# Kernel optimization log

Hardware: AMD Instinct MI355X
Metric: run time of the kernel (lower is better)

Reference implementation:

```python
import jax, jax.numpy as jnp
import numpy as np

B, D, TC, TE, TGT = 8, 256, 2048, 2048, 256
SCALE = 16.0  # sqrt(256.0) hardcoded in the original module


def setup_inputs() -> dict:
    key = jax.random.key(0)
    k1, k2, k3 = jax.random.split(key, 3)
    content_emb = jax.random.normal(k1, (B, D, TC), dtype=jnp.float32)
    emotion_emb = jax.random.normal(k2, (B, D, TE), dtype=jnp.float32)
    # Conv1d(embed_dim*2 -> target_embed, kernel=3): weight [out, in, k]
    fan_in = 2 * D * 3
    conv_w = jax.random.normal(k3, (TGT, 2 * D, 3), dtype=jnp.float32) / np.sqrt(fan_in)
    conv_b = jnp.zeros((TGT,), dtype=jnp.float32)
    return {"content_emb": content_emb, "emotion_emb": emotion_emb,
            "conv_w": conv_w, "conv_b": conv_b}


def reference(content_emb, emotion_emb, conv_w, conv_b):
    # (B, D, T) -> (B, T, D)
    c = jnp.transpose(content_emb, (0, 2, 1))   # [B, Tc, D]
    e = jnp.transpose(emotion_emb, (0, 2, 1))   # [B, Te, D]
    sim = jnp.einsum('btd,bsd->bts', c, e)      # [B, Tc, Te]
    attn = jax.nn.softmax(sim / SCALE, axis=-1)
    weighted_emo = jnp.einsum('bts,bsd->btd', attn, e)  # [B, Tc, D]
    x = jnp.concatenate([c, weighted_emo], axis=-1)     # [B, Tc, 2D]
    x = jnp.transpose(x, (0, 2, 1))                     # [B, 2D, Tc]
    out = jax.lax.conv_general_dilated(
        x, conv_w, window_strides=(1,), padding=[(1, 1)],
        dimension_numbers=('NCH', 'OIH', 'NCH'))
    return out + conv_b[None, :, None]
```

## Files before the change

### kernel.cpp

```cpp
#include <hip/hip_runtime.h>

typedef __bf16 bf16x8 __attribute__((ext_vector_type(8)));
typedef __bf16 bf16x4 __attribute__((ext_vector_type(4)));
typedef float  f32x4  __attribute__((ext_vector_type(4)));

#define MFMA(a, b, c) __builtin_amdgcn_mfma_f32_16x16x32_bf16((a), (b), (c), 0, 0, 0)
#define DRAIN_VMCNT() __builtin_amdgcn_s_waitcnt(0x0F70)

constexpr int Bc  = 8;
constexpr int D   = 256;
constexpr int TC  = 2048;
constexpr int TE  = 2048;
constexpr int TGT = 256;
constexpr int XR  = 256;
constexpr int NBT = Bc * TC;

#define EXP_C 0.09016844005556021f

__device__ __forceinline__ void gl_lds16(const __bf16* g, __bf16* l) {
  __builtin_amdgcn_global_load_lds(
      (const __attribute__((address_space(1))) void*)g,
      (__attribute__((address_space(3))) void*)l, 16, 0, 0);
}

__global__ void k_prep_all(const float* __restrict__ content,
                           const float* __restrict__ emotion,
                           __bf16* __restrict__ xcat,
                           __bf16* __restrict__ e_t, __bf16* __restrict__ e_ds,
                           const float* __restrict__ w, __bf16* __restrict__ Wk) {
  __shared__ __bf16 tile[64][68];
  const int tid = threadIdx.x;

  if (blockIdx.x == TC / 64) {
    const int base = (blockIdx.y * Bc + blockIdx.z) * 2048;
#pragma unroll
    for (int j = 0; j < 8; ++j) {
      const int idx = base + j * 256 + tid;
      const int o = idx >> 9, i = idx & 511;
#pragma unroll
      for (int k = 0; k < 3; ++k)
        Wk[k * (TGT * 512) + idx] = (__bf16)w[(size_t)o * 1536 + i * 3 + k];
    }
    return;
  }

  const bool isC = blockIdx.y < 4;
  const int b  = blockIdx.z;
  const int t0 = blockIdx.x * 64;
  const int d0 = (blockIdx.y & 3) * 64;
  const int c4 = (tid & 15) * 4;
  const int r0 = tid >> 4;
  const float* sp = (isC ? content : emotion) + ((size_t)b * D + d0) * 2048 + t0;
  __bf16* dsp = e_ds + ((size_t)b * D + d0) * TE + t0;
#pragma unroll
  for (int i = 0; i < 4; ++i) {
    const int r = r0 + 16 * i;
    const float4 v = *(const float4*)(sp + (size_t)r * 2048 + c4);
    bf16x4 pv;
    pv[0] = (__bf16)v.x; pv[1] = (__bf16)v.y; pv[2] = (__bf16)v.z; pv[3] = (__bf16)v.w;
    *(bf16x4*)&tile[r][c4] = pv;
    if (!isC) *(bf16x4*)(dsp + (size_t)r * TE + c4) = pv;
  }
  __syncthreads();
  __bf16* dp = (isC ? xcat + ((size_t)b * TC + t0) * XR
                    : e_t + ((size_t)b * TE + t0) * D) + d0;
#pragma unroll
  for (int i = 0; i < 2; ++i) {
    const int idx = tid + 256 * i;
    const int r   = idx >> 3;
    const int c8  = (idx & 7) * 8;
    bf16x8 v;
#pragma unroll
    for (int j = 0; j < 8; ++j) v[j] = tile[c8 + j][r];
    *(bf16x8*)(dp + (size_t)r * 256 + c8) = v;
  }
}

__global__ __launch_bounds__(256, 2) void k_attn(const __bf16* __restrict__ xcat,
                                                 const __bf16* __restrict__ e_t,
                                                 const __bf16* __restrict__ e_ds,
                                                 __bf16* __restrict__ Op,
                                                 float* __restrict__ Lp) {
  __shared__ __align__(16) __bf16 sEt[2][8192];
  __shared__ __align__(16) __bf16 sEs[2][8192];
  __shared__ __align__(16) __bf16 sP[4][2][640];

  const int tid  = threadIdx.x;
  const int lane = tid & 63;
  const int w    = tid >> 6;
  const int q    = lane >> 4;
  const int tl   = lane & 15;
  const int b    = blockIdx.y;
  const int z    = blockIdx.z;
  const int tbase = blockIdx.x * 128 + w * 32;

  const __bf16* etb = e_t  + (size_t)b * TE * D;
  const __bf16* esb = e_ds + (size_t)b * D * TE;

  bf16x8 cB[2][8];
#pragma unroll
  for (int tt = 0; tt < 2; ++tt) {
    const __bf16* crow = xcat + ((size_t)(b * TC) + tbase + tt * 16 + tl) * XR + q * 8;
#pragma unroll
    for (int ks = 0; ks < 8; ++ks) cB[tt][ks] = *(const bf16x8*)(crow + ks * 32);
  }

  unsigned offEt[4], offEs[4];
#pragma unroll
  for (int c = 0; c < 4; ++c) {
    const int id = (w * 4 + c) * 64 + lane;
    const int ss = id >> 5, cs = id & 31;
    offEt[c] = ss * D + (cs ^ (ss & 7)) * 8;
    const int dd = id >> 2, ps = id & 3;
    offEs[c] = dd * TE + (ps ^ ((dd >> 2) & 3)) * 8;
  }

  f32x4 accO[2][16];
#pragma unroll
  for (int tt = 0; tt < 2; ++tt)
#pragma unroll
    for (int dt = 0; dt < 16; ++dt) accO[tt][dt] = (f32x4){0.f, 0.f, 0.f, 0.f};
  float lacc[2] = {0.f, 0.f};

  const int sbase = z * (TE / 4);
  const int sw3 = (tl >> 2) & 3;

  auto stage = [&](int buf, int s0) {
#pragma unroll
    for (int c = 0; c < 4; ++c) {
      gl_lds16(etb + (size_t)s0 * D + offEt[c], &sEt[buf][(w * 4 + c) * 512]);
      gl_lds16(esb + s0 + offEs[c], &sEs[buf][(w * 4 + c) * 512]);
    }
  };

  stage(0, sbase);
  DRAIN_VMCNT();
  __syncthreads();

  int cur = 0;
  for (int k = 0; k < TE / 128; ++k) {
    if (k < TE / 128 - 1) stage(cur ^ 1, sbase + (k + 1) * 32);

    f32x4 aS[2][2];
#pragma unroll
    for (int i = 0; i < 2; ++i)
#pragma unroll
      for (int j = 0; j < 2; ++j) aS[i][j] = (f32x4){0.f, 0.f, 0.f, 0.f};
    const __bf16* pe = &sEt[cur][0];
#pragma unroll
    for (int ks = 0; ks < 8; ++ks) {
      const int ch = (ks * 4 + q) ^ (tl & 7);
      bf16x8 a0 = *(const bf16x8*)(pe + (tl * 32 + ch) * 8);
      bf16x8 a1 = *(const bf16x8*)(pe + ((16 + tl) * 32 + ch) * 8);
      aS[0][0] = MFMA(a0, cB[0][ks], aS[0][0]);
      aS[0][1] = MFMA(a0, cB[1][ks], aS[0][1]);
      aS[1][0] = MFMA(a1, cB[0][ks], aS[1][0]);
      aS[1][1] = MFMA(a1, cB[1][ks], aS[1][1]);
    }

#pragma unroll
    for (int tt = 0; tt < 2; ++tt) {
      bf16x4 w0, w1;
#pragma unroll
      for (int r = 0; r < 4; ++r) {
        float e0 = exp2f(aS[0][tt][r] * EXP_C);
        float e1 = exp2f(aS[1][tt][r] * EXP_C);
        lacc[tt] += e0 + e1;
        w0[r] = (__bf16)e0;
        w1[r] = (__bf16)e1;
      }
      __bf16* pw = &sP[w][tt][tl * 40 + q * 4];
      *(bf16x4*)pw = w0;
      *(bf16x4*)(pw + 16) = w1;
    }
    bf16x8 pB0 = *(const bf16x8*)(&sP[w][0][tl * 40 + q * 8]);
    bf16x8 pB1 = *(const bf16x8*)(&sP[w][1][tl * 40 + q * 8]);

    const __bf16* ps = &sEs[cur][0];
#pragma unroll
    for (int dt = 0; dt < 16; ++dt) {
      bf16x8 a = *(const bf16x8*)(ps + ((dt * 16 + tl) * 4 + (q ^ sw3)) * 8);
      accO[0][dt] = MFMA(a, pB0, accO[0][dt]);
      accO[1][dt] = MFMA(a, pB1, accO[1][dt]);
    }

    DRAIN_VMCNT();
    __syncthreads();
    cur ^= 1;
  }

#pragma unroll
  for (int tt = 0; tt < 2; ++tt) {
    float v = lacc[tt];
    v += __shfl_xor(v, 16, 64);
    v += __shfl_xor(v, 32, 64);
    const size_t row = (size_t)z * NBT + b * TC + tbase + tt * 16 + tl;
    if (q == 0) Lp[row] = v;
    __bf16* orow = Op + row * D + q * 4;
#pragma unroll
    for (int dt = 0; dt < 16; ++dt) {
      bf16x4 o;
#pragma unroll
      for (int r = 0; r < 4; ++r) o[r] = (__bf16)accO[tt][dt][r];
      *(bf16x4*)(orow + dt * 16) = o;
    }
  }
}

__global__ __launch_bounds__(256, 2) void k_conv(const __bf16* __restrict__ xcat,
                                                 const __bf16* __restrict__ Op,
                                                 const float* __restrict__ Lp,
                                                 const __bf16* __restrict__ Wk,
                                                 const float* __restrict__ bias,
                                                 float* __restrict__ out) {
  __shared__ __align__(16) __bf16 sXA[34 * 256];
  __shared__ __align__(16) __bf16 sXB[34 * 256];
  __shared__ __align__(16) __bf16 sW[2][8192];
  const int tid  = threadIdx.x;
  const int lane = tid & 63;
  const int wv   = tid >> 6;
  const int q    = lane >> 4;
  const int tl   = lane & 15;
  const int b    = blockIdx.x & 7;
  const int t0   = (blockIdx.x >> 3) * 32;
  const int o0   = wv * 64;
  const int sw3  = (tl >> 2) & 3;
  const int rh   = lane >> 5;
  const int l5   = lane & 31;

  const __bf16* xb = xcat + (size_t)b * TC * XR;
  for (int i = wv; i < 17; i += 4) {
    const int rl = 2 * i + rh;
    int gr = t0 - 1 + rl;
    gr = gr < 0 ? 0 : (gr > TC - 1 ? TC - 1 : gr);
    const int cs = l5 ^ (rl & 7);
    gl_lds16(xb + (size_t)gr * XR + cs * 8, &sXA[i * 512]);
  }

  unsigned offW[4];
#pragma unroll
  for (int c = 0; c < 4; ++c) {
    const int id = (wv * 4 + c) * 64 + lane;
    const int o = id >> 2, ps = id & 3;
    offW[c] = o * 512 + (ps ^ ((o >> 2) & 3)) * 8;
  }
  auto stageW = [&](int buf, int s) {
    const int kk = s >> 4, is = s & 15;
    const __bf16* wb = Wk + (size_t)kk * TGT * 512 + is * 32;
#pragma unroll
    for (int c = 0; c < 4; ++c)
      gl_lds16(wb + offW[c], &sW[buf][(wv * 4 + c) * 512]);
  };
  stageW(0, 0);

  for (int i = wv; i < 17; i += 4) {
    const int rl = 2 * i + rh;
    int gr = t0 - 1 + rl;
    gr = gr < 0 ? 0 : (gr > TC - 1 ? TC - 1 : gr);
    const size_t row = (size_t)b * TC + gr;
    const float inv = 1.0f /
        (Lp[row] + Lp[NBT + row] + Lp[2 * NBT + row] + Lp[3 * NBT + row]);
    float a8[8] = {0.f, 0.f, 0.f, 0.f, 0.f, 0.f, 0.f, 0.f};
#pragma unroll
    for (int zz = 0; zz < 4; ++zz) {
      bf16x8 a = *(const bf16x8*)(Op + ((size_t)zz * NBT + row) * D + l5 * 8);
#pragma unroll
      for (int r = 0; r < 8; ++r) a8[r] += (float)a[r];
    }
    bf16x8 o;
#pragma unroll
    for (int r = 0; r < 8; ++r) o[r] = (__bf16)(a8[r] * inv);
    *(bf16x8*)((char*)&sXB[rl * 256] + ((l5 * 16) ^ ((rl & 7) << 4))) = o;
  }

  DRAIN_VMCNT();
  __syncthreads();

  if (t0 == 0) {
    sXA[tid] = (__bf16)0.f; sXB[tid] = (__bf16)0.f;
    __syncthreads();
  }
  if (t0 + 32 == TC) {
    sXA[33 * 256 + tid] = (__bf16)0.f; sXB[33 * 256 + tid] = (__bf16)0.f;
    __syncthreads();
  }

  f32x4 acc[4][2];
#pragma unroll
  for (int mt = 0; mt < 4; ++mt) {
#pragma unroll
    for (int r = 0; r < 4; ++r) {
      const float bv = bias[o0 + mt * 16 + q * 4 + r];
#pragma unroll
      for (int nt = 0; nt < 2; ++nt) acc[mt][nt][r] = bv;
    }
  }

  int cur = 0;
  for (int s = 0; s < 48; ++s) {
    if (s < 47) stageW(cur ^ 1, s + 1);
    const int kk = s >> 4, is = s & 15;
    const __bf16* pl = (is & 8) ? sXB : sXA;
    const int cbyte = (is & 7) * 64 + q * 16;
    bf16x8 bfr[2];
#pragma unroll
    for (int nt = 0; nt < 2; ++nt) {
      const int t = nt * 16 + tl + kk;
      bfr[nt] = *(const bf16x8*)((const char*)pl + t * 512 + (cbyte ^ ((t & 7) << 4)));
    }
#pragma unroll
    for (int mt = 0; mt < 4; ++mt) {
      const int o = o0 + mt * 16 + tl;
      bf16x8 af = *(const bf16x8*)(&sW[cur][(o * 4 + (q ^ sw3)) * 8]);
#pragma unroll
      for (int nt = 0; nt < 2; ++nt) acc[mt][nt] = MFMA(af, bfr[nt], acc[mt][nt]);
    }
    DRAIN_VMCNT();
    __syncthreads();
    cur ^= 1;
  }

#pragma unroll
  for (int mt = 0; mt < 4; ++mt) {
#pragma unroll
    for (int nt = 0; nt < 2; ++nt) {
#pragma unroll
      for (int r = 0; r < 4; ++r) {
        const int o = o0 + mt * 16 + q * 4 + r;
        const int t = t0 + nt * 16 + tl;
        out[((size_t)b * TGT + o) * TC + t] = acc[mt][nt][r];
      }
    }
  }
}

extern "C" void kernel_launch(void* const* d_in, const int* in_sizes, int n_in,
                              void* d_out, int out_size, void* d_ws, size_t ws_size,
                              hipStream_t stream) {
  (void)in_sizes; (void)n_in; (void)out_size; (void)ws_size;
  const float* content = (const float*)d_in[0];
  const float* emotion = (const float*)d_in[1];
  const float* conv_w  = (const float*)d_in[2];
  const float* conv_b  = (const float*)d_in[3];
  float* out = (float*)d_out;

  char* ws = (char*)d_ws;
  __bf16* xcat = (__bf16*)ws;
  __bf16* Wk   = (__bf16*)(ws + 8388608);
  __bf16* Op   = (__bf16*)(ws + 9437184);
  float*  Lp   = (float*)(ws + 42991616);
  __bf16* e_t  = (__bf16*)d_out;
  __bf16* e_ds = (__bf16*)((char*)d_out + 8388608);

  k_prep_all<<<dim3(TC / 64 + 1, 8, Bc), 256, 0, stream>>>(
      content, emotion, xcat, e_t, e_ds, conv_w, Wk);
  k_attn<<<dim3(TC / 128, Bc, 4), 256, 0, stream>>>(xcat, e_t, e_ds, Op, Lp);
  k_conv<<<dim3((TC / 32) * Bc), 256, 0, stream>>>(xcat, Op, Lp, Wk, conv_b, out);
}
```

Baseline: 179.3 us.

## Store emotion d-major copy in 32-column blocked layout and interleave batch in grid

Measured after the change: 171.5 us. 4.3% less time.

```diff
diff --git a/kernel.cpp b/kernel.cpp
--- a/kernel.cpp
+++ b/kernel.cpp
@@ -26,7 +26,7 @@
 __global__ void k_prep_all(const float* __restrict__ content,
                            const float* __restrict__ emotion,
                            __bf16* __restrict__ xcat,
-                           __bf16* __restrict__ e_t, __bf16* __restrict__ e_ds,
+                           __bf16* __restrict__ e_t, __bf16* __restrict__ e_ds2,
                            const float* __restrict__ w, __bf16* __restrict__ Wk) {
   __shared__ __bf16 tile[64][68];
   const int tid = threadIdx.x;
@@ -51,7 +51,6 @@
   const int c4 = (tid & 15) * 4;
   const int r0 = tid >> 4;
   const float* sp = (isC ? content : emotion) + ((size_t)b * D + d0) * 2048 + t0;
-  __bf16* dsp = e_ds + ((size_t)b * D + d0) * TE + t0;
 #pragma unroll
   for (int i = 0; i < 4; ++i) {
     const int r = r0 + 16 * i;
@@ -59,9 +58,9 @@
     bf16x4 pv;
     pv[0] = (__bf16)v.x; pv[1] = (__bf16)v.y; pv[2] = (__bf16)v.z; pv[3] = (__bf16)v.w;
     *(bf16x4*)&tile[r][c4] = pv;
-    if (!isC) *(bf16x4*)(dsp + (size_t)r * TE + c4) = pv;
   }
   __syncthreads();
+
   __bf16* dp = (isC ? xcat + ((size_t)b * TC + t0) * XR
                     : e_t + ((size_t)b * TE + t0) * D) + d0;
 #pragma unroll
@@ -74,11 +73,26 @@
     for (int j = 0; j < 8; ++j) v[j] = tile[c8 + j][r];
     *(bf16x8*)(dp + (size_t)r * 256 + c8) = v;
   }
+
+  if (!isC) {
+    const int row = tid >> 2, sc = tid & 3;
+#pragma unroll
+    for (int h = 0; h < 2; ++h) {
+      bf16x4 lo = *(const bf16x4*)&tile[row][h * 32 + sc * 8];
+      bf16x4 hi = *(const bf16x4*)&tile[row][h * 32 + sc * 8 + 4];
+      bf16x8 v;
+      v[0] = lo[0]; v[1] = lo[1]; v[2] = lo[2]; v[3] = lo[3];
+      v[4] = hi[0]; v[5] = hi[1]; v[6] = hi[2]; v[7] = hi[3];
+      __bf16* qp = e_ds2 +
+          ((((size_t)b * 64 + (t0 >> 5) + h) * 256 + d0 + row) << 5) + sc * 8;
+      *(bf16x8*)qp = v;
+    }
+  }
 }
 
 __global__ __launch_bounds__(256, 2) void k_attn(const __bf16* __restrict__ xcat,
                                                  const __bf16* __restrict__ e_t,
-                                                 const __bf16* __restrict__ e_ds,
+                                                 const __bf16* __restrict__ e_ds2,
                                                  __bf16* __restrict__ Op,
                                                  float* __restrict__ Lp) {
   __shared__ __align__(16) __bf16 sEt[2][8192];
@@ -90,12 +104,13 @@
   const int w    = tid >> 6;
   const int q    = lane >> 4;
   const int tl   = lane & 15;
-  const int b    = blockIdx.y;
+  const int b    = blockIdx.x & 7;
+  const int xt   = (blockIdx.x >> 3) | (blockIdx.y << 1);
   const int z    = blockIdx.z;
-  const int tbase = blockIdx.x * 128 + w * 32;
-
-  const __bf16* etb = e_t  + (size_t)b * TE * D;
-  const __bf16* esb = e_ds + (size_t)b * D * TE;
+  const int tbase = xt * 128 + w * 32;
+
+  const __bf16* etb  = e_t  + (size_t)b * TE * D;
+  const __bf16* esb2 = e_ds2 + (size_t)b * 64 * 8192;
 
   bf16x8 cB[2][8];
 #pragma unroll
@@ -112,7 +127,7 @@
     const int ss = id >> 5, cs = id & 31;
     offEt[c] = ss * D + (cs ^ (ss & 7)) * 8;
     const int dd = id >> 2, ps = id & 3;
-    offEs[c] = dd * TE + (ps ^ ((dd >> 2) & 3)) * 8;
+    offEs[c] = dd * 32 + (ps ^ ((dd >> 2) & 3)) * 8;
   }
 
   f32x4 accO[2][16];
@@ -126,10 +141,12 @@
   const int sw3 = (tl >> 2) & 3;
 
   auto stage = [&](int buf, int s0) {
+    const __bf16* et = etb + (size_t)s0 * D;
+    const __bf16* es = esb2 + ((size_t)(s0 >> 5)) * 8192;
 #pragma unroll
     for (int c = 0; c < 4; ++c) {
-      gl_lds16(etb + (size_t)s0 * D + offEt[c], &sEt[buf][(w * 4 + c) * 512]);
-      gl_lds16(esb + s0 + offEs[c], &sEs[buf][(w * 4 + c) * 512]);
+      gl_lds16(et + offEt[c], &sEt[buf][(w * 4 + c) * 512]);
+      gl_lds16(es + offEs[c], &sEs[buf][(w * 4 + c) * 512]);
     }
   };
 
@@ -349,11 +366,11 @@
   __bf16* Wk   = (__bf16*)(ws + 8388608);
   __bf16* Op   = (__bf16*)(ws + 9437184);
   float*  Lp   = (float*)(ws + 42991616);
-  __bf16* e_t  = (__bf16*)d_out;
-  __bf16* e_ds = (__bf16*)((char*)d_out + 8388608);
+  __bf16* e_t   = (__bf16*)d_out;
+  __bf16* e_ds2 = (__bf16*)((char*)d_out + 8388608);
 
   k_prep_all<<<dim3(TC / 64 + 1, 8, Bc), 256, 0, stream>>>(
-      content, emotion, xcat, e_t, e_ds, conv_w, Wk);
-  k_attn<<<dim3(TC / 128, Bc, 4), 256, 0, stream>>>(xcat, e_t, e_ds, Op, Lp);
+      content, emotion, xcat, e_t, e_ds2, conv_w, Wk);
+  k_attn<<<dim3(TC / 128, Bc, 4), 256, 0, stream>>>(xcat, e_t, e_ds2, Op, Lp);
   k_conv<<<dim3((TC / 32) * Bc), 256, 0, stream>>>(xcat, Op, Lp, Wk, conv_b, out);
 }
```
